# Kernel tuning notes

Hardware: AMD Instinct MI355X
Metric: run time of the kernel (lower is better)

The kernel has to match this reference:

```python
import jax, jax.numpy as jnp
import numpy as np

B, N, D = 8, 256, 16   # batch, set size, in_dim
HID = 256              # hidden width (hidden_dims[:-1])
H = 128                # attention feature dim (hidden_dims[-1])
DH = 64                # per-dim feature dim d_h
NH = 4                 # attention heads


def _made_masks():
    in_deg = np.arange(1, D + 1)
    h_deg = (np.arange(HID) % (D - 1)) + 1
    out_deg = np.repeat(in_deg, H)  # per-dim contiguous layout -> reshape(..., D, H)
    m0 = h_deg[None, :] >= in_deg[:, None]
    m1 = h_deg[None, :] >= h_deg[:, None]
    m2 = out_deg[None, :] > h_deg[:, None]
    return jnp.array(m0), jnp.array(m1), jnp.array(m2)


def setup_inputs() -> dict:
    key = jax.random.key(0)
    ks = iter(jax.random.split(key, 40))
    def w(fi, fo):
        return jax.random.normal(next(ks), (fi, fo), jnp.float32) / np.sqrt(fi)
    inp = {"t": jnp.array([0.5], jnp.float32),
           "x": jax.random.normal(next(ks), (B, N, D), jnp.float32)}
    qd = [D, HID, HID, H * D]
    kd = [D, HID, HID, H]
    dd = [DH + 2, HID, HID, H, 1]
    for i in range(3):
        inp[f"q_w{i}"] = w(qd[i], qd[i + 1]); inp[f"q_b{i}"] = jnp.zeros((qd[i + 1],), jnp.float32)
        inp[f"k_w{i}"] = w(kd[i], kd[i + 1]); inp[f"k_b{i}"] = jnp.zeros((kd[i + 1],), jnp.float32)
        inp[f"v_w{i}"] = w(kd[i], kd[i + 1]); inp[f"v_b{i}"] = jnp.zeros((kd[i + 1],), jnp.float32)
    inp["p_w"] = w(H, DH); inp["p_b"] = jnp.zeros((DH,), jnp.float32)
    for i in range(4):
        inp[f"d_w{i}"] = w(dd[i], dd[i + 1]); inp[f"d_b{i}"] = jnp.zeros((dd[i + 1],), jnp.float32)
    inp["q_m0"], inp["q_m1"], inp["q_m2"] = _made_masks()
    return inp


def reference(t, x, q_w0, q_b0, k_w0, k_b0, v_w0, v_b0, q_w1, q_b1, k_w1, k_b1, v_w1, v_b1,
              q_w2, q_b2, k_w2, k_b2, v_w2, v_b2, p_w, p_b,
              d_w0, d_b0, d_w1, d_b1, d_w2, d_b2, d_w3, d_b3, q_m0, q_m1, q_m2):
    # --- exclusive net: MADE query (hollow per dim), MLP key/value, diagonal-masked attention ---
    hq = jax.nn.relu(x @ (q_w0 * q_m0) + q_b0)
    hq = jax.nn.relu(hq @ (q_w1 * q_m1) + q_b1)
    q = (hq @ (q_w2 * q_m2) + q_b2).reshape(B, N, D, H)      # [B,N,D,H]

    def mlp3(z, w0, b0, w1, b1, w2, b2):
        z = jnp.tanh(z @ w0 + b0)
        z = jnp.tanh(z @ w1 + b1)
        return z @ w2 + b2

    k = mlp3(x, k_w0, k_b0, k_w1, k_b1, k_w2, k_b2)          # [B,N,H] (shared across dims)
    v = mlp3(x, v_w0, v_b0, v_w1, v_b1, v_w2, v_b2)          # [B,N,H]

    dh = H // NH
    qh = q.transpose(0, 2, 1, 3).reshape(B, D, N, NH, dh).transpose(0, 1, 3, 2, 4)  # [B,D,NH,N,dh]
    kh = k.reshape(B, N, NH, dh).transpose(0, 2, 1, 3)        # [B,NH,N,dh]
    vh = v.reshape(B, N, NH, dh).transpose(0, 2, 1, 3)

    # einsum avoids materializing the repeat_interleaved key/value (same math)
    scores = jnp.einsum('bdhnc,bhmc->bdhnm', qh, kh) / np.sqrt(dh)
    scores = jnp.where(jnp.eye(N, dtype=bool), -jnp.inf, scores)  # mask self-attention (hollow)
    att = jax.nn.softmax(scores, axis=-1)
    o = jnp.einsum('bdhnm,bhmc->bdhnc', att, vh)              # [B,D,NH,N,dh]
    o = o.transpose(0, 1, 3, 2, 4).reshape(B, D, N, H).transpose(0, 2, 1, 3)  # [B,N,D,H]
    hfeat = o @ p_w + p_b                                     # [B,N,D,DH], hollow wrt x[...,d]

    # --- dimwise net: y_d = MLP([t, x_d, h_d]); exact diagonal Jacobian via jvp on x channel ---
    tb = jnp.broadcast_to(t.reshape(()), (B, N, D, 1)).astype(x.dtype)
    def dimwise(xc):
        z = jnp.concatenate([tb, xc, hfeat], -1)              # [B,N,D,2+DH]
        z = jnp.tanh(z @ d_w0 + d_b0)
        z = jnp.tanh(z @ d_w1 + d_b1)
        z = jnp.tanh(z @ d_w2 + d_b2)
        return (z @ d_w3 + d_b3)[..., 0]                      # [B,N,D]

    y, jac = jax.jvp(dimwise, (x[..., None],), (jnp.ones((B, N, D, 1), x.dtype),))
    return y, jac
```

## Files before the change

kernel.cpp:

```cpp
#include <hip/hip_runtime.h>
#include <hip/hip_bf16.h>

constexpr int kB = 8, kN = 256, kD = 16, kHID = 256, kH = 128, kDH = 64, kdh = 32;
constexpr int kBN = kB * kN;
constexpr int kP  = kBN * kD;

__device__ __forceinline__ float b2f(__hip_bfloat16 v) { return __bfloat162float(v); }
__device__ __forceinline__ __hip_bfloat16 f2b(float v) { return __float2bfloat16(v); }
__device__ __forceinline__ unsigned short f2bs(float v) {
    __hip_bfloat16 h = __float2bfloat16(v);
    return *(unsigned short*)&h;
}

__device__ __forceinline__ float tanh_fast(float v) {
    float e = __expf(2.f * v);
    return 1.f - 2.f * __builtin_amdgcn_rcpf(e + 1.f);
}

typedef short s8v  __attribute__((ext_vector_type(8)));
typedef float f4v  __attribute__((ext_vector_type(4)));
#define MFMA(a, b, c) __builtin_amdgcn_mfma_f32_16x16x32_bf16((a), (b), (c), 0, 0, 0)

__global__ __launch_bounds__(256) void prep_frag(
    const float* p_w, const float* d_w0, const float* d_w1, const float* d_w2,
    const float* k_w0, const float* k_w1, const float* k_w2,
    const float* v_w0, const float* v_w1, const float* v_w2,
    const float* q_w0, const float* q_w1, const float* q_w2,
    __hip_bfloat16* pwf, __hip_bfloat16* w0f, __hip_bfloat16* w1f, __hip_bfloat16* w2f,
    __hip_bfloat16* k0f, __hip_bfloat16* k1f, __hip_bfloat16* k2f,
    __hip_bfloat16* v0f, __hip_bfloat16* v1f, __hip_bfloat16* v2f,
    __hip_bfloat16* q0f, __hip_bfloat16* q1f, __hip_bfloat16* q2f)
{
    const int tile = blockIdx.x * 4 + (threadIdx.x >> 6);
    const int lane = threadIdx.x & 63;
    const float* src; __hip_bfloat16* dst; int N, NT, local, Kreal = 1 << 30, mask = 0;
    if (tile < 16)        { src = p_w;        dst = pwf; N = 64;   NT = 4;   local = tile; }
    else if (tile < 48)   { src = d_w0 + 512; dst = w0f; N = 256;  NT = 16;  local = tile - 16; }
    else if (tile < 176)  { src = d_w1;       dst = w1f; N = 256;  NT = 16;  local = tile - 48; }
    else if (tile < 240)  { src = d_w2;       dst = w2f; N = 128;  NT = 8;   local = tile - 176; }
    else if (tile < 256)  { src = k_w0;       dst = k0f; N = 256;  NT = 16;  local = tile - 240; Kreal = 16; }
    else if (tile < 272)  { src = v_w0;       dst = v0f; N = 256;  NT = 16;  local = tile - 256; Kreal = 16; }
    else if (tile < 288)  { src = q_w0;       dst = q0f; N = 256;  NT = 16;  local = tile - 272; Kreal = 16; mask = 1; }
    else if (tile < 416)  { src = k_w1;       dst = k1f; N = 256;  NT = 16;  local = tile - 288; }
    else if (tile < 544)  { src = v_w1;       dst = v1f; N = 256;  NT = 16;  local = tile - 416; }
    else if (tile < 672)  { src = q_w1;       dst = q1f; N = 256;  NT = 16;  local = tile - 544; mask = 2; }
    else if (tile < 736)  { src = k_w2;       dst = k2f; N = 128;  NT = 8;   local = tile - 672; }
    else if (tile < 800)  { src = v_w2;       dst = v2f; N = 128;  NT = 8;   local = tile - 736; }
    else                  { src = q_w2;       dst = q2f; N = 2048; NT = 128; local = tile - 800; mask = 3; }
    const int kt = local / NT, nt = local % NT;
    const int row0 = kt * 32 + (lane >> 4) * 8;
    const int col  = nt * 16 + (lane & 15);
    __hip_bfloat16* o = dst + ((size_t)local * 64 + lane) * 8;
    #pragma unroll
    for (int j = 0; j < 8; ++j) {
        const int r = row0 + j;
        float w = (r < Kreal) ? src[(size_t)r * N + col] : 0.f;
        if (mask == 1 && !((col % 15) >= r))        w = 0.f;
        if (mask == 2 && !((col % 15) >= (r % 15))) w = 0.f;
        if (mask == 3 && !((col >> 7) > (r % 15)))  w = 0.f;
        o[j] = f2b(w);
    }
}

__global__ __launch_bounds__(256) void mlp_kernel(
    const float* x,
    const float* k_b0, const float* k_b1, const float* k_b2,
    const float* v_b0, const float* v_b1, const float* v_b2,
    const float* q_b0, const float* q_b1,
    const __hip_bfloat16* k0f, const __hip_bfloat16* k1f, const __hip_bfloat16* k2f,
    const __hip_bfloat16* v0f, const __hip_bfloat16* v1f, const __hip_bfloat16* v2f,
    const __hip_bfloat16* q0f, const __hip_bfloat16* q1f,
    __hip_bfloat16* kbuf, __hip_bfloat16* vbuf, __hip_bfloat16* h1q)
{
    constexpr int SA = 264;
    constexpr int SX = 40;
    __shared__ __hip_bfloat16 xin[32 * SX];
    __shared__ __hip_bfloat16 bufA[32 * SA];
    __shared__ __hip_bfloat16 bufB[32 * SA];

    const int tid  = threadIdx.x;
    const int wv   = tid >> 6, lane = tid & 63;
    const int lx   = lane & 15, quad = lane >> 4;
    const int r0   = blockIdx.x * 32;

    auto ldA = [&](const __hip_bfloat16* buf, int stride, int m0, int k0) -> s8v {
        return *(const s8v*)(buf + (m0 + lx) * stride + k0 + quad * 8);
    };
    auto ldB = [&](const __hip_bfloat16* wf, int NT, int kt, int nt) -> s8v {
        return *(const s8v*)(wf + (((size_t)(kt * NT + nt) * 64 + lane) << 3));
    };

    for (int idx = tid; idx < 1024; idx += 256) {
        const int row = idx >> 5, c = idx & 31;
        xin[row * SX + c] = f2b(c < 16 ? x[(r0 + row) * kD + c] : 0.f);
    }

    const __hip_bfloat16* F0[3] = { k0f, v0f, q0f };
    const __hip_bfloat16* F1[3] = { k1f, v1f, q1f };
    const __hip_bfloat16* F2[2] = { k2f, v2f };
    const float* Ba0[3] = { k_b0, v_b0, q_b0 };
    const float* Ba1[3] = { k_b1, v_b1, q_b1 };
    const float* Ba2[2] = { k_b2, v_b2 };
    __hip_bfloat16* O2[2] = { kbuf, vbuf };

    for (int path = 0; path < 3; ++path) {
        __syncthreads();

        {
            f4v acc[4][2] = {};
            const s8v a0 = ldA(xin, SX, 0, 0);
            const s8v a1 = ldA(xin, SX, 16, 0);
            #pragma unroll
            for (int j = 0; j < 4; ++j) {
                s8v b = ldB(F0[path], 16, 0, wv * 4 + j);
                acc[j][0] = MFMA(a0, b, acc[j][0]);
                acc[j][1] = MFMA(a1, b, acc[j][1]);
            }
            #pragma unroll
            for (int j = 0; j < 4; ++j) {
                const int n = (wv * 4 + j) * 16 + lx;
                const float bb = Ba0[path][n];
                #pragma unroll
                for (int mt = 0; mt < 2; ++mt)
                #pragma unroll
                for (int r = 0; r < 4; ++r) {
                    const float v = acc[j][mt][r] + bb;
                    const float z = (path == 2) ? fmaxf(v, 0.f) : tanh_fast(v);
                    bufA[(mt * 16 + quad * 4 + r) * SA + n] = f2b(z);
                }
            }
        }
        __syncthreads();

        {
            f4v acc[4][2] = {};
            #pragma unroll
            for (int kt = 0; kt < 8; ++kt) {
                const s8v a0 = ldA(bufA, SA, 0, kt * 32);
                const s8v a1 = ldA(bufA, SA, 16, kt * 32);
                #pragma unroll
                for (int j = 0; j < 4; ++j) {
                    s8v b = ldB(F1[path], 16, kt, wv * 4 + j);
                    acc[j][0] = MFMA(a0, b, acc[j][0]);
                    acc[j][1] = MFMA(a1, b, acc[j][1]);
                }
            }
            #pragma unroll
            for (int j = 0; j < 4; ++j) {
                const int n = (wv * 4 + j) * 16 + lx;
                const float bb = Ba1[path][n];
                #pragma unroll
                for (int mt = 0; mt < 2; ++mt)
                #pragma unroll
                for (int r = 0; r < 4; ++r) {
                    const int m = mt * 16 + quad * 4 + r;
                    const float v = acc[j][mt][r] + bb;
                    if (path == 2) {
                        h1q[(size_t)(r0 + m) * 256 + n] = f2b(fmaxf(v, 0.f));
                    } else {
                        bufB[m * SA + n] = f2b(tanh_fast(v));
                    }
                }
            }
        }
        if (path == 2) break;
        __syncthreads();

        {
            f4v acc[2][2] = {};
            #pragma unroll
            for (int kt = 0; kt < 8; ++kt) {
                const s8v a0 = ldA(bufB, SA, 0, kt * 32);
                const s8v a1 = ldA(bufB, SA, 16, kt * 32);
                #pragma unroll
                for (int j = 0; j < 2; ++j) {
                    s8v b = ldB(F2[path], 8, kt, wv * 2 + j);
                    acc[j][0] = MFMA(a0, b, acc[j][0]);
                    acc[j][1] = MFMA(a1, b, acc[j][1]);
                }
            }
            #pragma unroll
            for (int j = 0; j < 2; ++j) {
                const int n = (wv * 2 + j) * 16 + lx;
                const float bb = Ba2[path][n];
                #pragma unroll
                for (int mt = 0; mt < 2; ++mt)
                #pragma unroll
                for (int r = 0; r < 4; ++r) {
                    const int m = mt * 16 + quad * 4 + r;
                    O2[path][(size_t)(r0 + m) * kH + n] = f2b(acc[j][mt][r] + bb);
                }
            }
        }
    }
}

__global__ __launch_bounds__(256) void qgemm_kernel(
    const float* q_b2, const __hip_bfloat16* h1q, const __hip_bfloat16* q2f,
    __hip_bfloat16* qbuf)
{
    constexpr int SA = 264;
    __shared__ __hip_bfloat16 hin[32 * SA];

    const int tid  = threadIdx.x;
    const int wv   = tid >> 6, lane = tid & 63;
    const int lx   = lane & 15, quad = lane >> 4;
    const int ct   = blockIdx.x & 7;
    const int r0   = (blockIdx.x >> 3) * 32;

    for (int idx = tid; idx < 1024; idx += 256) {
        const int row = idx >> 5, seg = idx & 31;
        *(f4v*)(hin + row * SA + seg * 8) = *(const f4v*)(h1q + (size_t)(r0 + row) * 256 + seg * 8);
    }
    __syncthreads();

    f4v acc[4][2] = {};
    #pragma unroll
    for (int kt = 0; kt < 8; ++kt) {
        const s8v a0 = *(const s8v*)(hin + lx * SA + kt * 32 + quad * 8);
        const s8v a1 = *(const s8v*)(hin + (16 + lx) * SA + kt * 32 + quad * 8);
        #pragma unroll
        for (int j = 0; j < 4; ++j) {
            s8v b = *(const s8v*)(q2f + (((size_t)(kt * 128 + ct * 16 + wv * 4 + j) * 64 + lane) << 3));
            acc[j][0] = MFMA(a0, b, acc[j][0]);
            acc[j][1] = MFMA(a1, b, acc[j][1]);
        }
    }
    const float scale = 0.17677669529663687f;
    #pragma unroll
    for (int j = 0; j < 4; ++j) {
        const int col = ct * 256 + (wv * 4 + j) * 16 + lx;
        const float bb = q_b2[col];
        #pragma unroll
        for (int mt = 0; mt < 2; ++mt)
        #pragma unroll
        for (int r = 0; r < 4; ++r) {
            const int row = r0 + mt * 16 + quad * 4 + r;
            qbuf[(size_t)row * 2048 + col] = f2b((acc[j][mt][r] + bb) * scale);
        }
    }
}

__global__ __launch_bounds__(256, 2) void attn_kernel(
    const __hip_bfloat16* qbuf, const __hip_bfloat16* kbuf, const __hip_bfloat16* vbuf,
    float* obuf)
{
    constexpr int SP = 264;
    __shared__ short Pl[4][16 * SP];

    const int blk = blockIdx.x;
    const int hd = blk & 3;
    const int d  = (blk >> 2) & 15;
    const int b  = blk >> 6;

    const int wv   = threadIdx.x >> 6;
    const int lane = threadIdx.x & 63;
    const int lx = lane & 15, quad = lane >> 4;
    short* Pw = &Pl[wv][0];

    const short* kb = (const short*)kbuf;
    const short* vb = (const short*)vbuf;
    const short* qb = (const short*)qbuf;

    s8v kfrag[16];
    #pragma unroll
    for (int mt = 0; mt < 16; ++mt)
        kfrag[mt] = *(const s8v*)(kb + (size_t)(b * 256 + mt * 16 + lx) * 128 + hd * 32 + quad * 8);

    s8v vfrag[2][8];
    #pragma unroll
    for (int ntv = 0; ntv < 2; ++ntv)
    #pragma unroll
    for (int kt = 0; kt < 8; ++kt) {
        s8v v;
        #pragma unroll
        for (int j = 0; j < 8; ++j)
            v[j] = vb[(size_t)(b * 256 + kt * 32 + quad * 8 + j) * 128 + hd * 32 + ntv * 16 + lx];
        vfrag[ntv][kt] = v;
    }

    const float LOG2E = 1.4426950408889634f;

    for (int mi = 0; mi < 4; ++mi) {
        const int q0 = wv * 64 + mi * 16;

        s8v qfrag = *(const s8v*)(qb + (size_t)(b * 256 + q0 + lx) * 2048 + d * 128 + hd * 32 + quad * 8);

        f4v acc[16];
        #pragma unroll
        for (int mt = 0; mt < 16; ++mt) acc[mt] = f4v{0.f, 0.f, 0.f, 0.f};
        #pragma unroll
        for (int mt = 0; mt < 16; ++mt) acc[mt] = MFMA(kfrag[mt], qfrag, acc[mt]);

        const int qg = q0 + lx;
        float mx = -3.0e38f;
        #pragma unroll
        for (int mt = 0; mt < 16; ++mt)
        #pragma unroll
        for (int r = 0; r < 4; ++r) {
            const int key = mt * 16 + quad * 4 + r;
            float s = (key == qg) ? -3.0e38f : acc[mt][r];
            acc[mt][r] = s;
            mx = fmaxf(mx, s);
        }
        mx = fmaxf(mx, __shfl_xor(mx, 16, 64));
        mx = fmaxf(mx, __shfl_xor(mx, 32, 64));

        const float nmxc = -mx * LOG2E;
        float l = 0.f;
        #pragma unroll
        for (int mt = 0; mt < 16; ++mt)
        #pragma unroll
        for (int r = 0; r < 4; ++r) {
            float p = exp2f(__builtin_fmaf(acc[mt][r], LOG2E, nmxc));
            acc[mt][r] = p;
            l += p;
        }
        l += __shfl_xor(l, 16, 64);
        l += __shfl_xor(l, 32, 64);

        #pragma unroll
        for (int mt = 0; mt < 16; ++mt) {
            unsigned short h0 = f2bs(acc[mt][0]);
            unsigned short h1 = f2bs(acc[mt][1]);
            unsigned short h2 = f2bs(acc[mt][2]);
            unsigned short h3 = f2bs(acc[mt][3]);
            uint2 w;
            w.x = (unsigned int)h0 | ((unsigned int)h1 << 16);
            w.y = (unsigned int)h2 | ((unsigned int)h3 << 16);
            *(uint2*)(Pw + lx * SP + mt * 16 + quad * 4) = w;
        }
        __asm__ volatile("s_waitcnt lgkmcnt(0)" ::: "memory");

        f4v av[2] = { f4v{0.f,0.f,0.f,0.f}, f4v{0.f,0.f,0.f,0.f} };
        #pragma unroll
        for (int kt = 0; kt < 8; ++kt) {
            s8v a = *(const s8v*)(Pw + lx * SP + kt * 32 + quad * 8);
            av[0] = MFMA(a, vfrag[0][kt], av[0]);
            av[1] = MFMA(a, vfrag[1][kt], av[1]);
        }
        __asm__ volatile("s_waitcnt lgkmcnt(0)" ::: "memory");

        #pragma unroll
        for (int r = 0; r < 4; ++r) {
            const float lr = __shfl(l, quad * 4 + r, 64);
            const float inv = __builtin_amdgcn_rcpf(lr);
            const int qrow = q0 + quad * 4 + r;
            #pragma unroll
            for (int ntv = 0; ntv < 2; ++ntv) {
                obuf[((size_t)((b * 256 + qrow) * 16 + d)) * 128 + hd * 32 + ntv * 16 + lx]
                    = av[ntv][r] * inv;
            }
        }
    }
}

__global__ __launch_bounds__(256) void dim_kernel(
    const float* t, const float* x,
    const float* p_b, const float* d_w0, const float* d_b0,
    const float* d_b1, const float* d_b2, const float* d_w3, const float* d_b3,
    const __hip_bfloat16* pwf, const __hip_bfloat16* w0f,
    const __hip_bfloat16* w1f, const __hip_bfloat16* w2f,
    const float* obuf, float* out)
{
    constexpr int SA = 264;
    constexpr int SO = 136;
    constexpr int SH = 72;
    __shared__ __hip_bfloat16 bufA[64 * SA];
    __shared__ __hip_bfloat16 bufB[64 * SA];
    __shared__ float xvs[32];

    const int tid  = threadIdx.x;
    const int wv   = tid >> 6, lane = tid & 63;
    const int lx   = lane & 15, quad = lane >> 4;
    const int p0   = blockIdx.x * 32;
    const float tval = t[0];

    auto ldA = [&](const __hip_bfloat16* buf, int stride, int m0, int k0) -> s8v {
        return *(const s8v*)(buf + (m0 + lx) * stride + k0 + quad * 8);
    };
    auto ldBf = [&](const __hip_bfloat16* wf, int NT, int kt, int nt) -> s8v {
        return *(const s8v*)(wf + (((size_t)(kt * NT + nt) * 64 + lane) << 3));
    };

    for (int idx = tid; idx < 1024; idx += 256) {
        const int row = idx >> 5, seg = idx & 31;
        f4v v = *(const f4v*)(obuf + (size_t)(p0 + row) * kH + seg * 4);
        __hip_bfloat16* dst = bufA + row * SO + seg * 4;
        dst[0] = f2b(v[0]); dst[1] = f2b(v[1]); dst[2] = f2b(v[2]); dst[3] = f2b(v[3]);
    }
    if (tid < 32) xvs[tid] = x[p0 + tid];
    __syncthreads();

    {
        f4v acc0 = {}, acc1 = {};
        #pragma unroll
        for (int ktile = 0; ktile < 4; ++ktile) {
            s8v b  = ldBf(pwf, 4, ktile, wv);
            s8v a0 = ldA(bufA, SO, 0,  ktile * 32);
            s8v a1 = ldA(bufA, SO, 16, ktile * 32);
            acc0 = MFMA(a0, b, acc0);
            acc1 = MFMA(a1, b, acc1);
        }
        const int n = wv * 16 + lx;
        const float bb = p_b[n];
        #pragma unroll
        for (int r = 0; r < 4; ++r) {
            bufB[(quad * 4 + r) * SH + n]        = f2b(acc0[r] + bb);
            bufB[(16 + quad * 4 + r) * SH + n]   = f2b(acc1[r] + bb);
        }
    }
    __syncthreads();

    {
        f4v acc[4][2] = {};
        #pragma unroll
        for (int ktile = 0; ktile < 2; ++ktile) {
            s8v a0 = ldA(bufB, SH, 0,  ktile * 32);
            s8v a1 = ldA(bufB, SH, 16, ktile * 32);
            #pragma unroll
            for (int j = 0; j < 4; ++j) {
                s8v b = ldBf(w0f, 16, ktile, wv * 4 + j);
                acc[j][0] = MFMA(a0, b, acc[j][0]);
                acc[j][1] = MFMA(a1, b, acc[j][1]);
            }
        }
        #pragma unroll
        for (int j = 0; j < 4; ++j) {
            const int n = (wv * 4 + j) * 16 + lx;
            const float base = d_b0[n] + tval * d_w0[n];
            const float wx   = d_w0[256 + n];
            #pragma unroll
            for (int mt = 0; mt < 2; ++mt)
            #pragma unroll
            for (int r = 0; r < 4; ++r) {
                const int m = mt * 16 + quad * 4 + r;
                const float z = tanh_fast(acc[j][mt][r] + base + xvs[m] * wx);
                bufA[m * SA + n]        = f2b(z);
                bufA[(m + 32) * SA + n] = f2b((1.f - z * z) * wx);
            }
        }
    }
    __syncthreads();

    {
        f4v acc[4][4] = {};
        #pragma unroll
        for (int ktile = 0; ktile < 8; ++ktile) {
            s8v a[4];
            #pragma unroll
            for (int mt = 0; mt < 4; ++mt) a[mt] = ldA(bufA, SA, mt * 16, ktile * 32);
            #pragma unroll
            for (int j = 0; j < 4; ++j) {
                s8v b = ldBf(w1f, 16, ktile, wv * 4 + j);
                #pragma unroll
                for (int mt = 0; mt < 4; ++mt) acc[j][mt] = MFMA(a[mt], b, acc[j][mt]);
            }
        }
        #pragma unroll
        for (int j = 0; j < 4; ++j) {
            const int n = (wv * 4 + j) * 16 + lx;
            const float b1 = d_b1[n];
            #pragma unroll
            for (int mt = 0; mt < 2; ++mt)
            #pragma unroll
            for (int r = 0; r < 4; ++r) {
                const int m = mt * 16 + quad * 4 + r;
                const float z  = tanh_fast(acc[j][mt][r] + b1);
                const float zd = (1.f - z * z) * acc[j][mt + 2][r];
                bufB[m * SA + n]        = f2b(z);
                bufB[(m + 32) * SA + n] = f2b(zd);
            }
        }
    }
    __syncthreads();

    {
        f4v acc[2][4] = {};
        #pragma unroll
        for (int ktile = 0; ktile < 8; ++ktile) {
            s8v a[4];
            #pragma unroll
            for (int mt = 0; mt < 4; ++mt) a[mt] = ldA(bufB, SA, mt * 16, ktile * 32);
            #pragma unroll
            for (int j = 0; j < 2; ++j) {
                s8v b = ldBf(w2f, 8, ktile, wv * 2 + j);
                #pragma unroll
                for (int mt = 0; mt < 4; ++mt) acc[j][mt] = MFMA(a[mt], b, acc[j][mt]);
            }
        }
        #pragma unroll
        for (int j = 0; j < 2; ++j) {
            const int n = (wv * 2 + j) * 16 + lx;
            const float b2 = d_b2[n];
            #pragma unroll
            for (int mt = 0; mt < 2; ++mt)
            #pragma unroll
            for (int r = 0; r < 4; ++r) {
                const int m = mt * 16 + quad * 4 + r;
                const float z  = tanh_fast(acc[j][mt][r] + b2);
                const float zd = (1.f - z * z) * acc[j][mt + 2][r];
                bufA[m * SO + n]        = f2b(z);
                bufA[(m + 32) * SO + n] = f2b(zd);
            }
        }
    }
    __syncthreads();

    {
        const int p = tid >> 3, s = tid & 7;
        float yv = 0.f, jv = 0.f;
        #pragma unroll
        for (int i = 0; i < 16; ++i) {
            const int n = s + i * 8;
            const float w = d_w3[n];
            yv += b2f(bufA[p * SO + n]) * w;
            jv += b2f(bufA[(p + 32) * SO + n]) * w;
        }
        #pragma unroll
        for (int off = 4; off > 0; off >>= 1) {
            yv += __shfl_down(yv, off, 8);
            jv += __shfl_down(jv, off, 8);
        }
        if (s == 0) {
            out[p0 + p]      = yv + d_b3[0];
            out[kP + p0 + p] = jv;
        }
    }
}

extern "C" void kernel_launch(void* const* d_in, const int* in_sizes, int n_in,
                              void* d_out, int out_size, void* d_ws, size_t ws_size,
                              hipStream_t stream)
{
    typedef const float* fp;
    fp t    = (fp)d_in[0];
    fp x    = (fp)d_in[1];
    fp q_w0 = (fp)d_in[2],  q_b0 = (fp)d_in[3];
    fp k_w0 = (fp)d_in[4],  k_b0 = (fp)d_in[5];
    fp v_w0 = (fp)d_in[6],  v_b0 = (fp)d_in[7];
    fp q_w1 = (fp)d_in[8],  q_b1 = (fp)d_in[9];
    fp k_w1 = (fp)d_in[10], k_b1 = (fp)d_in[11];
    fp v_w1 = (fp)d_in[12], v_b1 = (fp)d_in[13];
    fp q_w2 = (fp)d_in[14], q_b2 = (fp)d_in[15];
    fp k_w2 = (fp)d_in[16], k_b2 = (fp)d_in[17];
    fp v_w2 = (fp)d_in[18], v_b2 = (fp)d_in[19];
    fp p_w  = (fp)d_in[20], p_b  = (fp)d_in[21];
    fp d_w0 = (fp)d_in[22], d_b0 = (fp)d_in[23];
    fp d_w1 = (fp)d_in[24], d_b1 = (fp)d_in[25];
    fp d_w2 = (fp)d_in[26], d_b2 = (fp)d_in[27];
    fp d_w3 = (fp)d_in[28], d_b3 = (fp)d_in[29];

    float* obuf = (float*)d_ws;
    __hip_bfloat16* wsb  = (__hip_bfloat16*)(obuf + (size_t)kP * kH);
    __hip_bfloat16* kbuf = wsb;
    __hip_bfloat16* vbuf = kbuf + (size_t)kBN * kH;
    __hip_bfloat16* qbuf = vbuf + (size_t)kBN * kH;
    __hip_bfloat16* pwf  = qbuf + (size_t)kBN * kD * kH;
    __hip_bfloat16* w0f  = pwf + 8192;
    __hip_bfloat16* w1f  = w0f + 16384;
    __hip_bfloat16* w2f  = w1f + 65536;
    __hip_bfloat16* k0f  = w2f + 32768;
    __hip_bfloat16* v0f  = k0f + 8192;
    __hip_bfloat16* q0f  = v0f + 8192;
    __hip_bfloat16* k1f  = q0f + 8192;
    __hip_bfloat16* v1f  = k1f + 65536;
    __hip_bfloat16* q1f  = v1f + 65536;
    __hip_bfloat16* k2f  = q1f + 65536;
    __hip_bfloat16* v2f  = k2f + 32768;
    __hip_bfloat16* q2f  = v2f + 32768;
    __hip_bfloat16* h1q  = q2f + 524288;

    float* out = (float*)d_out;

    prep_frag<<<456, 256, 0, stream>>>(p_w, d_w0, d_w1, d_w2,
        k_w0, k_w1, k_w2, v_w0, v_w1, v_w2, q_w0, q_w1, q_w2,
        pwf, w0f, w1f, w2f, k0f, k1f, k2f, v0f, v1f, v2f, q0f, q1f, q2f);
    mlp_kernel<<<kBN / 32, 256, 0, stream>>>(x,
        k_b0, k_b1, k_b2, v_b0, v_b1, v_b2, q_b0, q_b1,
        k0f, k1f, k2f, v0f, v1f, v2f, q0f, q1f, kbuf, vbuf, h1q);
    qgemm_kernel<<<(kBN / 32) * 8, 256, 0, stream>>>(q_b2, h1q, q2f, qbuf);
    attn_kernel<<<kB * kD * 4, 256, 0, stream>>>(qbuf, kbuf, vbuf, obuf);
    dim_kernel<<<kP / 32, 256, 0, stream>>>(t, x, p_b, d_w0, d_b0, d_b1, d_b2, d_w3, d_b3,
        pwf, w0f, w1f, w2f, obuf, out);
}
```

Baseline: 215.1 us.

## Fuse query output GEMM into MLP kernel and store attention output as bf16

Merges the separate query final-layer GEMM into the MLP kernel, so the ReLU hidden activations stay in shared memory and one launch plus the h1q round trip are removed. The attention output buffer changes from fp32 to bf16, halving its write and read traffic, and the dim kernel loads it with vector copies. The cost is that the large 2048-column q GEMM now runs in only 64 blocks, looping serially over 8 column groups, which cuts parallelism.

```diff
diff --git a/kernel.cpp b/kernel.cpp
--- a/kernel.cpp
+++ b/kernel.cpp
@@ -62,15 +62,15 @@
     }
 }
 
-__global__ __launch_bounds__(256) void mlp_kernel(
+__global__ __launch_bounds__(256) void mlpq_kernel(
     const float* x,
     const float* k_b0, const float* k_b1, const float* k_b2,
     const float* v_b0, const float* v_b1, const float* v_b2,
-    const float* q_b0, const float* q_b1,
+    const float* q_b0, const float* q_b1, const float* q_b2,
     const __hip_bfloat16* k0f, const __hip_bfloat16* k1f, const __hip_bfloat16* k2f,
     const __hip_bfloat16* v0f, const __hip_bfloat16* v1f, const __hip_bfloat16* v2f,
-    const __hip_bfloat16* q0f, const __hip_bfloat16* q1f,
-    __hip_bfloat16* kbuf, __hip_bfloat16* vbuf, __hip_bfloat16* h1q)
+    const __hip_bfloat16* q0f, const __hip_bfloat16* q1f, const __hip_bfloat16* q2f,
+    __hip_bfloat16* kbuf, __hip_bfloat16* vbuf, __hip_bfloat16* qbuf)
 {
     constexpr int SA = 264;
     constexpr int SX = 40;
@@ -155,18 +155,13 @@
                 for (int r = 0; r < 4; ++r) {
                     const int m = mt * 16 + quad * 4 + r;
                     const float v = acc[j][mt][r] + bb;
-                    if (path == 2) {
-                        h1q[(size_t)(r0 + m) * 256 + n] = f2b(fmaxf(v, 0.f));
-                    } else {
-                        bufB[m * SA + n] = f2b(tanh_fast(v));
-                    }
-                }
-            }
-        }
-        if (path == 2) break;
+                    bufB[m * SA + n] = f2b(path == 2 ? fmaxf(v, 0.f) : tanh_fast(v));
+                }
+            }
+        }
         __syncthreads();
 
-        {
+        if (path < 2) {
             f4v acc[2][2] = {};
             #pragma unroll
             for (int kt = 0; kt < 8; ++kt) {
@@ -191,59 +186,41 @@
                     O2[path][(size_t)(r0 + m) * kH + n] = f2b(acc[j][mt][r] + bb);
                 }
             }
-        }
-    }
-}
-
-__global__ __launch_bounds__(256) void qgemm_kernel(
-    const float* q_b2, const __hip_bfloat16* h1q, const __hip_bfloat16* q2f,
-    __hip_bfloat16* qbuf)
-{
-    constexpr int SA = 264;
-    __shared__ __hip_bfloat16 hin[32 * SA];
-
-    const int tid  = threadIdx.x;
-    const int wv   = tid >> 6, lane = tid & 63;
-    const int lx   = lane & 15, quad = lane >> 4;
-    const int ct   = blockIdx.x & 7;
-    const int r0   = (blockIdx.x >> 3) * 32;
-
-    for (int idx = tid; idx < 1024; idx += 256) {
-        const int row = idx >> 5, seg = idx & 31;
-        *(f4v*)(hin + row * SA + seg * 8) = *(const f4v*)(h1q + (size_t)(r0 + row) * 256 + seg * 8);
-    }
-    __syncthreads();
-
-    f4v acc[4][2] = {};
-    #pragma unroll
-    for (int kt = 0; kt < 8; ++kt) {
-        const s8v a0 = *(const s8v*)(hin + lx * SA + kt * 32 + quad * 8);
-        const s8v a1 = *(const s8v*)(hin + (16 + lx) * SA + kt * 32 + quad * 8);
-        #pragma unroll
-        for (int j = 0; j < 4; ++j) {
-            s8v b = *(const s8v*)(q2f + (((size_t)(kt * 128 + ct * 16 + wv * 4 + j) * 64 + lane) << 3));
-            acc[j][0] = MFMA(a0, b, acc[j][0]);
-            acc[j][1] = MFMA(a1, b, acc[j][1]);
-        }
-    }
-    const float scale = 0.17677669529663687f;
-    #pragma unroll
-    for (int j = 0; j < 4; ++j) {
-        const int col = ct * 256 + (wv * 4 + j) * 16 + lx;
-        const float bb = q_b2[col];
-        #pragma unroll
-        for (int mt = 0; mt < 2; ++mt)
-        #pragma unroll
-        for (int r = 0; r < 4; ++r) {
-            const int row = r0 + mt * 16 + quad * 4 + r;
-            qbuf[(size_t)row * 2048 + col] = f2b((acc[j][mt][r] + bb) * scale);
+        } else {
+            const float scale = 0.17677669529663687f;
+            for (int g = 0; g < 8; ++g) {
+                f4v acc[4][2] = {};
+                #pragma unroll
+                for (int kt = 0; kt < 8; ++kt) {
+                    const s8v a0 = ldA(bufB, SA, 0, kt * 32);
+                    const s8v a1 = ldA(bufB, SA, 16, kt * 32);
+                    #pragma unroll
+                    for (int j = 0; j < 4; ++j) {
+                        s8v b = ldB(q2f, 128, kt, g * 16 + wv * 4 + j);
+                        acc[j][0] = MFMA(a0, b, acc[j][0]);
+                        acc[j][1] = MFMA(a1, b, acc[j][1]);
+                    }
+                }
+                #pragma unroll
+                for (int j = 0; j < 4; ++j) {
+                    const int col = (g * 16 + wv * 4 + j) * 16 + lx;
+                    const float bb = q_b2[col];
+                    #pragma unroll
+                    for (int mt = 0; mt < 2; ++mt)
+                    #pragma unroll
+                    for (int r = 0; r < 4; ++r) {
+                        const int row = r0 + mt * 16 + quad * 4 + r;
+                        qbuf[(size_t)row * 2048 + col] = f2b((acc[j][mt][r] + bb) * scale);
+                    }
+                }
+            }
         }
     }
 }
 
 __global__ __launch_bounds__(256, 2) void attn_kernel(
     const __hip_bfloat16* qbuf, const __hip_bfloat16* kbuf, const __hip_bfloat16* vbuf,
-    float* obuf)
+    __hip_bfloat16* obuf)
 {
     constexpr int SP = 264;
     __shared__ short Pl[4][16 * SP];
@@ -349,7 +326,7 @@
             #pragma unroll
             for (int ntv = 0; ntv < 2; ++ntv) {
                 obuf[((size_t)((b * 256 + qrow) * 16 + d)) * 128 + hd * 32 + ntv * 16 + lx]
-                    = av[ntv][r] * inv;
+                    = f2b(av[ntv][r] * inv);
             }
         }
     }
@@ -361,7 +338,7 @@
     const float* d_b1, const float* d_b2, const float* d_w3, const float* d_b3,
     const __hip_bfloat16* pwf, const __hip_bfloat16* w0f,
     const __hip_bfloat16* w1f, const __hip_bfloat16* w2f,
-    const float* obuf, float* out)
+    const __hip_bfloat16* obuf, float* out)
 {
     constexpr int SA = 264;
     constexpr int SO = 136;
@@ -383,11 +360,9 @@
         return *(const s8v*)(wf + (((size_t)(kt * NT + nt) * 64 + lane) << 3));
     };
 
-    for (int idx = tid; idx < 1024; idx += 256) {
-        const int row = idx >> 5, seg = idx & 31;
-        f4v v = *(const f4v*)(obuf + (size_t)(p0 + row) * kH + seg * 4);
-        __hip_bfloat16* dst = bufA + row * SO + seg * 4;
-        dst[0] = f2b(v[0]); dst[1] = f2b(v[1]); dst[2] = f2b(v[2]); dst[3] = f2b(v[3]);
+    for (int idx = tid; idx < 512; idx += 256) {
+        const int row = idx >> 4, ch = idx & 15;
+        *(f4v*)(bufA + row * SO + ch * 8) = *(const f4v*)(obuf + (size_t)(p0 + row) * kH + ch * 8);
     }
     if (tid < 32) xvs[tid] = x[p0 + tid];
     __syncthreads();
@@ -536,7 +511,7 @@
     typedef const float* fp;
     fp t    = (fp)d_in[0];
     fp x    = (fp)d_in[1];
-    fp q_w0 = (fp)d_in[2],  q_b0 = (fp)d_in[3];
+    fp q_w0 = (fp)d_in[2],  fp_q_b0 = (fp)d_in[3];
     fp k_w0 = (fp)d_in[4],  k_b0 = (fp)d_in[5];
     fp v_w0 = (fp)d_in[6],  v_b0 = (fp)d_in[7];
     fp q_w1 = (fp)d_in[8],  q_b1 = (fp)d_in[9];
@@ -550,13 +525,14 @@
     fp d_w1 = (fp)d_in[24], d_b1 = (fp)d_in[25];
     fp d_w2 = (fp)d_in[26], d_b2 = (fp)d_in[27];
     fp d_w3 = (fp)d_in[28], d_b3 = (fp)d_in[29];
-
-    float* obuf = (float*)d_ws;
-    __hip_bfloat16* wsb  = (__hip_bfloat16*)(obuf + (size_t)kP * kH);
+    fp q_b0 = fp_q_b0;
+
+    __hip_bfloat16* wsb  = (__hip_bfloat16*)d_ws;
     __hip_bfloat16* kbuf = wsb;
     __hip_bfloat16* vbuf = kbuf + (size_t)kBN * kH;
     __hip_bfloat16* qbuf = vbuf + (size_t)kBN * kH;
-    __hip_bfloat16* pwf  = qbuf + (size_t)kBN * kD * kH;
+    __hip_bfloat16* obuf = qbuf + (size_t)kBN * kD * kH;
+    __hip_bfloat16* pwf  = obuf + (size_t)kP * kH;
     __hip_bfloat16* w0f  = pwf + 8192;
     __hip_bfloat16* w1f  = w0f + 16384;
     __hip_bfloat16* w2f  = w1f + 65536;
@@ -569,17 +545,15 @@
     __hip_bfloat16* k2f  = q1f + 65536;
     __hip_bfloat16* v2f  = k2f + 32768;
     __hip_bfloat16* q2f  = v2f + 32768;
-    __hip_bfloat16* h1q  = q2f + 524288;
 
     float* out = (float*)d_out;
 
     prep_frag<<<456, 256, 0, stream>>>(p_w, d_w0, d_w1, d_w2,
         k_w0, k_w1, k_w2, v_w0, v_w1, v_w2, q_w0, q_w1, q_w2,
         pwf, w0f, w1f, w2f, k0f, k1f, k2f, v0f, v1f, v2f, q0f, q1f, q2f);
-    mlp_kernel<<<kBN / 32, 256, 0, stream>>>(x,
-        k_b0, k_b1, k_b2, v_b0, v_b1, v_b2, q_b0, q_b1,
-        k0f, k1f, k2f, v0f, v1f, v2f, q0f, q1f, kbuf, vbuf, h1q);
-    qgemm_kernel<<<(kBN / 32) * 8, 256, 0, stream>>>(q_b2, h1q, q2f, qbuf);
+    mlpq_kernel<<<kBN / 32, 256, 0, stream>>>(x,
+        k_b0, k_b1, k_b2, v_b0, v_b1, v_b2, q_b0, q_b1, q_b2,
+        k0f, k1f, k2f, v0f, v1f, v2f, q0f, q1f, q2f, kbuf, vbuf, qbuf);
     attn_kernel<<<kB * kD * 4, 256, 0, stream>>>(qbuf, kbuf, vbuf, obuf);
     dim_kernel<<<kP / 32, 256, 0, stream>>>(t, x, p_b, d_w0, d_b0, d_b1, d_b2, d_w3, d_b3,
         pwf, w0f, w1f, w2f, obuf, out);
```

Result: slower. 242.5 us (+12.8%).
